# Kernel optimization log

Hardware: AMD Instinct MI355X
Metric: run time of the kernel (lower is better)

Reference implementation:

```python
import jax, jax.numpy as jnp
import numpy as np

N_M, N_H = 50000, 50000
E = 600000
D_IN, D_OUT = 128, 128
LN_EPS = 1e-5
NORM_EPS = 1e-12


def _segment_mean(x, seg, n):
    # PyG 'mean' aggregation: sum / count, 0 for isolated nodes (count clamped to 1)
    s = jax.ops.segment_sum(x, seg, num_segments=n)
    c = jax.ops.segment_sum(jnp.ones((seg.shape[0], 1), x.dtype), seg, num_segments=n)
    return s / jnp.maximum(c, 1.0)


def _sage(t_src, t_dst, ei, Wl, bl, Wr):
    # SAGEConv: lin_l(mean_j x_j) + lin_r(x_i), then L2-normalize rows
    agg = _segment_mean(t_src[ei[0]], ei[1], t_dst.shape[0])
    out = agg @ Wl + bl + t_dst @ Wr
    nrm = jnp.maximum(jnp.linalg.norm(out, axis=-1, keepdims=True), NORM_EPS)
    return out / nrm


def _layer_norm(x, g, b):
    mu = jnp.mean(x, axis=-1, keepdims=True)
    v = jnp.var(x, axis=-1, keepdims=True)
    return (x - mu) / jnp.sqrt(v + LN_EPS) * g + b


def setup_inputs() -> dict:
    key = jax.random.key(0)
    ks = jax.random.split(key, 24)
    r = lambda i, shape: jax.random.normal(ks[i], shape, dtype=jnp.float32) * 0.05
    inp = {
        'x_microbe': jax.random.normal(ks[0], (N_M, D_IN), dtype=jnp.float32),
        'x_host': jax.random.normal(ks[1], (N_H, D_IN), dtype=jnp.float32),
        # per-node-type linear transforms
        'W_nt_m': r(2, (D_IN, D_OUT)), 'b_nt_m': r(3, (D_OUT,)),
        'W_nt_h': r(4, (D_IN, D_OUT)), 'b_nt_h': r(5, (D_OUT,)),
        # SAGEConv params per edge type (lin_l has bias, lin_r has no bias)
        'Wl_mm': r(6, (D_OUT, D_OUT)), 'bl_mm': r(7, (D_OUT,)), 'Wr_mm': r(8, (D_OUT, D_OUT)),
        'Wl_mh': r(9, (D_OUT, D_OUT)), 'bl_mh': r(10, (D_OUT,)), 'Wr_mh': r(11, (D_OUT, D_OUT)),
        'Wl_hm': r(12, (D_OUT, D_OUT)), 'bl_hm': r(13, (D_OUT,)), 'Wr_hm': r(14, (D_OUT, D_OUT)),
        # LayerNorm affine params per node type
        'g_m': jnp.ones((D_OUT,), jnp.float32), 'be_m': jnp.zeros((D_OUT,), jnp.float32),
        'g_h': jnp.ones((D_OUT,), jnp.float32), 'be_h': jnp.zeros((D_OUT,), jnp.float32),
        # edge indices [2, E]: row0 = src, row1 = dst
        'ei_mm': jax.random.randint(ks[15], (2, E), 0, N_M, dtype=jnp.int32),
        'ei_mh': jnp.stack([jax.random.randint(ks[16], (E,), 0, N_M, dtype=jnp.int32),
                            jax.random.randint(ks[17], (E,), 0, N_H, dtype=jnp.int32)]),
        'ei_hm': jnp.stack([jax.random.randint(ks[18], (E,), 0, N_H, dtype=jnp.int32),
                            jax.random.randint(ks[19], (E,), 0, N_M, dtype=jnp.int32)]),
    }
    return inp


def reference(x_microbe, x_host, W_nt_m, b_nt_m, W_nt_h, b_nt_h,
              Wl_mm, bl_mm, Wr_mm, Wl_mh, bl_mh, Wr_mh, Wl_hm, bl_hm, Wr_hm,
              g_m, be_m, g_h, be_h, ei_mm, ei_mh, ei_hm):
    # per-type linear transforms
    t_m = x_microbe @ W_nt_m + b_nt_m
    t_h = x_host @ W_nt_h + b_nt_h
    # SAGEConv per edge type
    o_mm = _sage(t_m, t_m, ei_mm, Wl_mm, bl_mm, Wr_mm)  # microbe -> microbe
    o_mh = _sage(t_m, t_h, ei_mh, Wl_mh, bl_mh, Wr_mh)  # microbe -> host
    o_hm = _sage(t_h, t_m, ei_hm, Wl_hm, bl_hm, Wr_hm)  # host -> microbe
    # HeteroConv aggr='mean' over edge types per dst node type
    conv_m = 0.5 * (o_mm + o_hm)
    conv_h = o_mh
    # residual + LayerNorm (dropout is identity in eval mode)
    out_m = _layer_norm(t_m + conv_m, g_m, be_m)
    out_h = _layer_norm(t_h + conv_h, g_h, be_h)
    return out_m, out_h
```

## Files before the change

### kernel.cpp

```cpp
#include <hip/hip_runtime.h>

typedef unsigned short u16;
typedef unsigned int u32;
typedef __attribute__((ext_vector_type(8))) short bf16x8;
typedef __attribute__((ext_vector_type(4))) float f32x4;

__device__ __forceinline__ float bf_lo(u32 u){ return __uint_as_float(u << 16); }
__device__ __forceinline__ float bf_hi(u32 u){ return __uint_as_float(u & 0xffff0000u); }
__device__ __forceinline__ float bf2f(u16 v){ return __uint_as_float((u32)v << 16); }
__device__ __forceinline__ u16 f2bf(float f){
    u32 u = __float_as_uint(f);
    u32 r = (u + 0x7fffu + ((u >> 16) & 1u)) >> 16;
    return (u16)r;
}
__device__ __forceinline__ u32 pack2(float a, float b){
    return (u32)f2bf(a) | ((u32)f2bf(b) << 16);
}

__global__ __launch_bounds__(256) void fusedA_kernel(
    const int* __restrict__ d0, const int* __restrict__ d1, const int* __restrict__ d2,
    int* __restrict__ rk0, int* __restrict__ rk1, int* __restrict__ rk2,
    int E0, int E1, int E2, int b0, int b1, int b2, int n0, int n1, int n2,
    int* __restrict__ cnt, int h0, int h1, int h2,
    const float* __restrict__ Wf0, const float* __restrict__ Wf1,
    const float* __restrict__ Wf2, const float* __restrict__ Wf3,
    const float* __restrict__ Wf4, const float* __restrict__ Wf5,
    u16* __restrict__ WF,
    const float* __restrict__ Xm, const float* __restrict__ Wm,
    const float* __restrict__ bm, u16* __restrict__ Tm, int NM,
    const float* __restrict__ Xh, const float* __restrict__ Wh,
    const float* __restrict__ bh, u16* __restrict__ Th, int NH,
    int gm, int gh)
{
    int bid = blockIdx.x;
    int HB = h0 + h1 + h2;
    if (bid < HB){
        int t, lb;
        if (bid < h0){ t = 0; lb = bid; }
        else if (bid < h0 + h1){ t = 1; lb = bid - h0; }
        else { t = 2; lb = bid - h0 - h1; }
        const int* d = t == 0 ? d0 : (t == 1 ? d1 : d2);
        int* rk = t == 0 ? rk0 : (t == 1 ? rk1 : rk2);
        int E = t == 0 ? E0 : (t == 1 ? E1 : E2);
        int b = t == 0 ? b0 : (t == 1 ? b1 : b2);
        int n = t == 0 ? n0 : (t == 1 ? n1 : n2);
        int i = lb * 256 + threadIdx.x;
        if (i < E){
            int x = d[i];
            if ((unsigned)x < (unsigned)n) rk[i] = atomicAdd(&cnt[b + x], 1);
        }
        return;
    }
    bid -= HB;
    if (bid < 6){
        const float* W = bid == 0 ? Wf0 : bid == 1 ? Wf1 : bid == 2 ? Wf2 :
                         bid == 3 ? Wf3 : bid == 4 ? Wf4 : Wf5;
        u16* dst = WF + (size_t)bid * 16384;
        #pragma unroll 4
        for (int k = 0; k < 64; ++k){
            int i = k * 256 + threadIdx.x;
            int j   = i & 7;
            int l16 = (i >> 3) & 15;
            int qd  = (i >> 7) & 3;
            int q   = (i >> 9) & 3;
            int tt  = (i >> 11) & 1;
            int w   = (i >> 12) & 3;
            dst[i] = f2bf(W[(q * 32 + qd * 8 + j) * 128 + (w * 32 + tt * 16 + l16)]);
        }
        return;
    }
    bid -= 6;
    const float *A, *W, *bias; u16* C; int N, lgrid, lbid;
    if (bid < gm){ A = Xm; W = Wm; bias = bm; C = Tm; N = NM; lgrid = gm; lbid = bid; }
    else         { A = Xh; W = Wh; bias = bh; C = Th; N = NH; lgrid = gh; lbid = bid - gm; }

    int tid = threadIdx.x;
    int wave = tid >> 6, lane = tid & 63;
    int colHalf = wave & 1;
    int ln16 = lane & 15, quad = lane >> 4;

    bf16x8 Bfrag[4][4];
    #pragma unroll
    for (int t = 0; t < 4; ++t){
        int col = colHalf * 64 + t * 16 + ln16;
        #pragma unroll
        for (int q = 0; q < 4; ++q){
            bf16x8 f;
            #pragma unroll
            for (int j = 0; j < 8; ++j)
                f[j] = (short)f2bf(W[(q * 32 + quad * 8 + j) * 128 + col]);
            Bfrag[t][q] = f;
        }
    }
    float bv[4];
    #pragma unroll
    for (int t = 0; t < 4; ++t)
        bv[t] = bias[colHalf * 64 + t * 16 + ln16];

    int rowBlocks = (N + 15) >> 4;
    for (int rb = lbid * 2 + (wave >> 1); rb < rowBlocks; rb += lgrid * 2){
        int row0 = rb * 16;
        int ar = row0 + ln16; if (ar > N - 1) ar = N - 1;
        const float* Arow = A + (size_t)ar * 128 + quad * 8;
        bf16x8 Af[4];
        #pragma unroll
        for (int q = 0; q < 4; ++q){
            f32x4 lo = *(const f32x4*)(Arow + q * 32);
            f32x4 hi = *(const f32x4*)(Arow + q * 32 + 4);
            bf16x8 f;
            #pragma unroll
            for (int j = 0; j < 4; ++j){ f[j] = (short)f2bf(lo[j]); f[4+j] = (short)f2bf(hi[j]); }
            Af[q] = f;
        }
        f32x4 acc[4];
        #pragma unroll
        for (int t = 0; t < 4; ++t) acc[t] = (f32x4){bv[t], bv[t], bv[t], bv[t]};
        #pragma unroll
        for (int q = 0; q < 4; ++q)
            #pragma unroll
            for (int t = 0; t < 4; ++t)
                acc[t] = __builtin_amdgcn_mfma_f32_16x16x32_bf16(Af[q], Bfrag[t][q], acc[t], 0, 0, 0);
        #pragma unroll
        for (int t = 0; t < 4; ++t){
            int col = colHalf * 64 + t * 16 + ln16;
            #pragma unroll
            for (int r = 0; r < 4; ++r){
                int row = row0 + quad * 4 + r;
                if (row < N) C[(size_t)row * 128 + col] = f2bf(acc[t][r]);
            }
        }
    }
}

__global__ __launch_bounds__(256) void scan_blocks_kernel(
    const int* __restrict__ cnt, int n, int* __restrict__ off, int* __restrict__ part)
{
    __shared__ int lds[256];
    int tid = threadIdx.x;
    int base = blockIdx.x * 2048 + tid * 8;
    int v[8]; int s = 0;
    #pragma unroll
    for (int j = 0; j < 8; ++j){
        int idx = base + j;
        int c = (idx < n) ? cnt[idx] : 0;
        v[j] = s; s += c;
    }
    lds[tid] = s;
    __syncthreads();
    for (int d = 1; d < 256; d <<= 1){
        int t = (tid >= d) ? lds[tid - d] : 0;
        __syncthreads();
        lds[tid] += t;
        __syncthreads();
    }
    int thrBase = (tid > 0) ? lds[tid - 1] : 0;
    if (tid == 255) part[blockIdx.x] = lds[255];
    #pragma unroll
    for (int j = 0; j < 8; ++j){
        int idx = base + j;
        if (idx < n) off[idx] = thrBase + v[j];
    }
}

__global__ __launch_bounds__(128) void scan_part_kernel(
    int* __restrict__ part, int np, int* __restrict__ total_slot)
{
    __shared__ int lds[128];
    int tid = threadIdx.x;
    lds[tid] = (tid < np) ? part[tid] : 0;
    __syncthreads();
    for (int d = 1; d < 128; d <<= 1){
        int t = (tid >= d) ? lds[tid - d] : 0;
        __syncthreads();
        lds[tid] += t;
        __syncthreads();
    }
    if (tid < np) part[tid] = (tid > 0) ? lds[tid - 1] : 0;
    if (tid == 0) *total_slot = lds[np - 1 < 0 ? 0 : np - 1];
}

__global__ __launch_bounds__(256) void scan_add_kernel(
    int* __restrict__ off, const int* __restrict__ part, int n)
{
    int i = blockIdx.x * 256 + threadIdx.x;
    if (i < n) off[i] += part[i >> 11];
}

__global__ __launch_bounds__(256) void fill3_kernel(
    const int* __restrict__ s0, const int* __restrict__ s1, const int* __restrict__ s2,
    const int* __restrict__ d0, const int* __restrict__ d1, const int* __restrict__ d2,
    const int* __restrict__ rk0, const int* __restrict__ rk1, const int* __restrict__ rk2,
    int E0, int E1, int E2, int b0, int b1, int b2, int n0, int n1, int n2,
    const int* __restrict__ off, int* __restrict__ slot)
{
    int t = blockIdx.y;
    int i = blockIdx.x * 256 + threadIdx.x;
    const int* sp = t == 0 ? s0 : (t == 1 ? s1 : s2);
    const int* dp = t == 0 ? d0 : (t == 1 ? d1 : d2);
    const int* rk = t == 0 ? rk0 : (t == 1 ? rk1 : rk2);
    int E = t == 0 ? E0 : (t == 1 ? E1 : E2);
    int b = t == 0 ? b0 : (t == 1 ? b1 : b2);
    int n = t == 0 ? n0 : (t == 1 ? n1 : n2);
    if (i < E){
        int x = dp[i];
        if ((unsigned)x < (unsigned)n){
            slot[off[b + x] + rk[i]] = sp[i];
        }
    }
}

template<int NT>
__global__ __launch_bounds__(256, 4) void sage_ln_kernel(
    const u16* __restrict__ Ts1, const u16* __restrict__ Ts2,
    const u16* __restrict__ Tdst,
    const int* __restrict__ off1, const int* __restrict__ off2,
    const int* __restrict__ slot, int ns1, int ns2,
    const u16* __restrict__ WFl1, const u16* __restrict__ WFr1, const float* __restrict__ bl1,
    const u16* __restrict__ WFl2, const u16* __restrict__ WFr2, const float* __restrict__ bl2,
    const float* __restrict__ g, const float* __restrict__ be,
    float* __restrict__ outp, int N, float scale)
{
    __shared__ u32 aggLDS[NT][16 * 68];
    __shared__ float redN[NT][4][16];
    __shared__ float redS[2][4][16];

    int tid = threadIdx.x;
    int wave = tid >> 6, lane = tid & 63;
    int ln16 = lane & 15, quad = lane >> 4;

    const u16* Ts[2] = {Ts1, Ts2};
    const int* offp[2] = {off1, off2};
    int nsv[2] = {ns1, ns2};
    const u16* WFl[2] = {WFl1, WFl2};
    const u16* WFr[2] = {WFr1, WFr2};
    const float* bls[2] = {bl1, bl2};

    float bv[NT][2];
    #pragma unroll
    for (int et = 0; et < NT; ++et)
        #pragma unroll
        for (int t = 0; t < 2; ++t)
            bv[et][t] = bls[et][wave * 32 + t * 16 + ln16];
    float gv[2], bev[2];
    #pragma unroll
    for (int t = 0; t < 2; ++t){
        int col = wave * 32 + t * 16 + ln16;
        gv[t] = g[col]; bev[t] = be[col];
    }

    int tiles = (N + 15) >> 4;
    for (int tile = blockIdx.x; tile < tiles; tile += gridDim.x){
        int row0 = tile * 16;

        #pragma unroll
        for (int et = 0; et < NT; ++et){
            const u16* Tsrc = Ts[et];
            const int* off = offp[et];
            int n_src = nsv[et];

            int rb[4], rdeg[4], rtake[4], myslot[4];
            #pragma unroll
            for (int r = 0; r < 4; ++r){
                int gg = row0 + wave * 4 + r;
                int b = 0, e = 0;
                if (gg < N){ b = off[gg]; e = off[gg + 1]; }
                rb[r] = b;
                int deg = e - b;
                rdeg[r] = deg;
                int take = deg < 64 ? deg : 64;
                rtake[r] = take;
                int s = 0;
                if (lane < take){
                    s = slot[b + lane];
                    if ((unsigned)s >= (unsigned)n_src) s = 0;
                }
                myslot[r] = s;
            }

            #pragma unroll
            for (int r = 0; r < 4; ++r){
                int lrow = wave * 4 + r;
                float p0 = 0.f, p1 = 0.f, q0 = 0.f, q1 = 0.f;
                float r0 = 0.f, r1 = 0.f, s0 = 0.f, s1 = 0.f;
                int take = rtake[r];
                int j = 0;
                for (; j + 4 <= take; j += 4){
                    int i0 = __shfl(myslot[r], j);
                    int i1 = __shfl(myslot[r], j + 1);
                    int i2 = __shfl(myslot[r], j + 2);
                    int i3 = __shfl(myslot[r], j + 3);
                    u32 u0 = *(const u32*)(Tsrc + (size_t)i0 * 128 + lane * 2);
                    u32 u1 = *(const u32*)(Tsrc + (size_t)i1 * 128 + lane * 2);
                    u32 u2 = *(const u32*)(Tsrc + (size_t)i2 * 128 + lane * 2);
                    u32 u3 = *(const u32*)(Tsrc + (size_t)i3 * 128 + lane * 2);
                    p0 += bf_lo(u0); p1 += bf_hi(u0);
                    q0 += bf_lo(u1); q1 += bf_hi(u1);
                    r0 += bf_lo(u2); r1 += bf_hi(u2);
                    s0 += bf_lo(u3); s1 += bf_hi(u3);
                }
                for (; j < take; ++j){
                    int i0 = __shfl(myslot[r], j);
                    u32 u0 = *(const u32*)(Tsrc + (size_t)i0 * 128 + lane * 2);
                    p0 += bf_lo(u0); p1 += bf_hi(u0);
                }
                for (int j2 = rb[r] + 64; j2 < rb[r] + rdeg[r]; ++j2){
                    int i0 = slot[j2];
                    if ((unsigned)i0 >= (unsigned)n_src) i0 = 0;
                    u32 u0 = *(const u32*)(Tsrc + (size_t)i0 * 128 + lane * 2);
                    p0 += bf_lo(u0); p1 += bf_hi(u0);
                }
                float a0 = (p0 + q0) + (r0 + s0);
                float a1 = (p1 + q1) + (r1 + s1);
                int c = rdeg[r] < 1 ? 1 : rdeg[r];
                float inv = 1.0f / (float)c;
                aggLDS[et][lrow * 68 + lane] = pack2(a0 * inv, a1 * inv);
            }
        }
        __syncthreads();

        int ar = row0 + ln16; if (ar > N - 1) ar = N - 1;
        const u16* Ar2 = Tdst + (size_t)ar * 128 + quad * 8;
        f32x4 acc[NT][2];
        #pragma unroll
        for (int et = 0; et < NT; ++et)
            #pragma unroll
            for (int t = 0; t < 2; ++t)
                acc[et][t] = (f32x4){bv[et][t], bv[et][t], bv[et][t], bv[et][t]};
        #pragma unroll
        for (int q = 0; q < 4; ++q){
            bf16x8 afr = *(const bf16x8*)(Ar2 + q * 32);
            #pragma unroll
            for (int et = 0; et < NT; ++et){
                bf16x8 afl = *(const bf16x8*)&aggLDS[et][ln16 * 68 + q * 16 + quad * 4];
                #pragma unroll
                for (int t = 0; t < 2; ++t){
                    int fo = ((((wave * 2 + t) * 4 + q) * 4 + quad) * 16 + ln16) * 8;
                    bf16x8 BLf = *(const bf16x8*)(WFl[et] + fo);
                    bf16x8 BRf = *(const bf16x8*)(WFr[et] + fo);
                    acc[et][t] = __builtin_amdgcn_mfma_f32_16x16x32_bf16(afl, BLf, acc[et][t], 0, 0, 0);
                    acc[et][t] = __builtin_amdgcn_mfma_f32_16x16x32_bf16(afr, BRf, acc[et][t], 0, 0, 0);
                }
            }
        }

        #pragma unroll
        for (int et = 0; et < NT; ++et){
            #pragma unroll
            for (int r = 0; r < 4; ++r){
                float s = acc[et][0][r] * acc[et][0][r] + acc[et][1][r] * acc[et][1][r];
                #pragma unroll
                for (int m = 1; m < 16; m <<= 1) s += __shfl_xor(s, m);
                if (ln16 == 0) redN[et][wave][quad * 4 + r] = s;
            }
        }
        __syncthreads();

        float yv[2][4];
        float lsum[4], lsq[4];
        #pragma unroll
        for (int r = 0; r < 4; ++r){
            int r16 = quad * 4 + r;
            int row = row0 + r16;
            int crow = row < N ? row : N - 1;
            float sc[NT];
            #pragma unroll
            for (int et = 0; et < NT; ++et){
                float tot = redN[et][0][r16] + redN[et][1][r16] + redN[et][2][r16] + redN[et][3][r16];
                sc[et] = scale / fmaxf(sqrtf(tot), 1e-12f);
            }
            float s1v = 0.f, s2v = 0.f;
            #pragma unroll
            for (int t = 0; t < 2; ++t){
                int col = wave * 32 + t * 16 + ln16;
                float y = bf2f(Tdst[(size_t)crow * 128 + col]);
                #pragma unroll
                for (int et = 0; et < NT; ++et) y += acc[et][t][r] * sc[et];
                yv[t][r] = y;
                s1v += y; s2v += y * y;
            }
            #pragma unroll
            for (int m = 1; m < 16; m <<= 1){ s1v += __shfl_xor(s1v, m); s2v += __shfl_xor(s2v, m); }
            lsum[r] = s1v; lsq[r] = s2v;
        }
        if (ln16 == 0){
            #pragma unroll
            for (int r = 0; r < 4; ++r){
                redS[0][wave][quad * 4 + r] = lsum[r];
                redS[1][wave][quad * 4 + r] = lsq[r];
            }
        }
        __syncthreads();

        #pragma unroll
        for (int r = 0; r < 4; ++r){
            int r16 = quad * 4 + r;
            int row = row0 + r16;
            if (row >= N) continue;
            float S1 = redS[0][0][r16] + redS[0][1][r16] + redS[0][2][r16] + redS[0][3][r16];
            float S2 = redS[1][0][r16] + redS[1][1][r16] + redS[1][2][r16] + redS[1][3][r16];
            float mean = S1 * (1.0f / 128.0f);
            float var = S2 * (1.0f / 128.0f) - mean * mean;
            float rstd = rsqrtf(var + 1e-5f);
            #pragma unroll
            for (int t = 0; t < 2; ++t){
                int col = wave * 32 + t * 16 + ln16;
                outp[(size_t)row * 128 + col] = (yv[t][r] - mean) * rstd * gv[t] + bev[t];
            }
        }
        __syncthreads();
    }
}

extern "C" void kernel_launch(void* const* d_in, const int* in_sizes, int n_in,
                              void* d_out, int out_size, void* d_ws, size_t ws_size,
                              hipStream_t stream) {
    const float* xm    = (const float*)d_in[0];
    const float* xh    = (const float*)d_in[1];
    const float* Wnt_m = (const float*)d_in[2];  const float* bnt_m = (const float*)d_in[3];
    const float* Wnt_h = (const float*)d_in[4];  const float* bnt_h = (const float*)d_in[5];
    const float* Wl_mm = (const float*)d_in[6];  const float* bl_mm = (const float*)d_in[7];
    const float* Wr_mm = (const float*)d_in[8];
    const float* Wl_mh = (const float*)d_in[9];  const float* bl_mh = (const float*)d_in[10];
    const float* Wr_mh = (const float*)d_in[11];
    const float* Wl_hm = (const float*)d_in[12]; const float* bl_hm = (const float*)d_in[13];
    const float* Wr_hm = (const float*)d_in[14];
    const float* g_m   = (const float*)d_in[15]; const float* be_m  = (const float*)d_in[16];
    const float* g_h   = (const float*)d_in[17]; const float* be_h  = (const float*)d_in[18];
    const int* ei_mm = (const int*)d_in[19];
    const int* ei_mh = (const int*)d_in[20];
    const int* ei_hm = (const int*)d_in[21];

    const int D = 128;
    const int NM = in_sizes[0] / D;
    const int NH = in_sizes[1] / D;
    const int E1 = in_sizes[19] / 2;
    const int E2 = in_sizes[20] / 2;
    const int E3 = in_sizes[21] / 2;
    const int Esum = E1 + E2 + E3;
    const int n3 = 2 * NM + NH;

    char* ws = (char*)d_ws;
    size_t woff = 0;
    auto alloc = [&](size_t bytes) -> void* {
        void* p = ws + woff;
        woff += (bytes + 255) & ~(size_t)255;
        return p;
    };
    u16* T_M   = (u16*)alloc((size_t)NM * D * 2);
    u16* T_H   = (u16*)alloc((size_t)NH * D * 2);
    int* CNT3  = (int*)alloc((size_t)n3 * 4);
    int* OFF3  = (int*)alloc((size_t)(n3 + 1) * 4);
    int* SLOT3 = (int*)alloc((size_t)Esum * 4);
    int* PART  = (int*)alloc(1024 * 4);
    u16* WF    = (u16*)alloc((size_t)6 * 16384 * 2);
    if (woff > ws_size) return;

    int* RANK3 = (int*)d_out;
    int* rk0 = RANK3, *rk1 = RANK3 + E1, *rk2 = RANK3 + E1 + E3;

    float* OUT_M = (float*)d_out;
    float* OUT_H = (float*)d_out + (size_t)NM * D;

    const int b0 = 0, b1 = NM, b2 = 2 * NM;
    const int h0 = (E1 + 255) / 256, h1 = (E3 + 255) / 256, h2 = (E2 + 255) / 256;
    const int gm = 1024, gh = 1024;
    int Emax = E1 > E2 ? E1 : E2; if (E3 > Emax) Emax = E3;
    const dim3 egrid((Emax + 255) / 256, 3);
    const int scanBlocks = (n3 + 2047) / 2048;

    hipMemsetAsync(CNT3, 0, (size_t)n3 * 4, stream);

    fusedA_kernel<<<h0 + h1 + h2 + 6 + gm + gh, 256, 0, stream>>>(
        ei_mm + E1, ei_hm + E3, ei_mh + E2,
        rk0, rk1, rk2,
        E1, E3, E2, b0, b1, b2, NM, NM, NH, CNT3, h0, h1, h2,
        Wl_mm, Wr_mm, Wl_hm, Wr_hm, Wl_mh, Wr_mh, WF,
        xm, Wnt_m, bnt_m, T_M, NM,
        xh, Wnt_h, bnt_h, T_H, NH, gm, gh);

    scan_blocks_kernel<<<scanBlocks, 256, 0, stream>>>(CNT3, n3, OFF3, PART);
    scan_part_kernel<<<1, 128, 0, stream>>>(PART, scanBlocks, OFF3 + n3);
    scan_add_kernel<<<(n3 + 255) / 256, 256, 0, stream>>>(OFF3, PART, n3);
    fill3_kernel<<<egrid, 256, 0, stream>>>(
        ei_mm, ei_hm, ei_mh,
        ei_mm + E1, ei_hm + E3, ei_mh + E2,
        rk0, rk1, rk2,
        E1, E3, E2, b0, b1, b2, NM, NM, NH, OFF3, SLOT3);

    sage_ln_kernel<2><<<(NM + 15) / 16, 256, 0, stream>>>(
        T_M, T_H, T_M, OFF3 + b0, OFF3 + b1, SLOT3, NM, NH,
        WF + 0 * 16384, WF + 1 * 16384, bl_mm,
        WF + 2 * 16384, WF + 3 * 16384, bl_hm,
        g_m, be_m, OUT_M, NM, 0.5f);
    sage_ln_kernel<1><<<(NH + 15) / 16, 256, 0, stream>>>(
        T_M, nullptr, T_H, OFF3 + b2, nullptr, SLOT3, NM, 0,
        WF + 4 * 16384, WF + 5 * 16384, bl_mh,
        nullptr, nullptr, nullptr,
        g_h, be_h, OUT_H, NH, 1.0f);
}
```

Before: 541.0 us.

## Split neighbor gather into separate kernel and preload weight fragments in GEMM-LN

The fused gather+GEMM+LayerNorm kernel is split in two. A grid-stride gather kernel computes mean-aggregated bf16 rows for all three edge types into global buffers (the host aggregate temporarily lives in the output buffer). A GEMM+LN kernel then reads those aggregates and keeps all weight fragments in registers, launched persistently with 1024 blocks. This trades an extra global round trip of the aggregates for better load balance, deeper gather unrolling and no LDS staging or barrier between gather and MFMA; register pressure from the preloaded weights may lower occupancy.

```diff
diff --git a/kernel.cpp b/kernel.cpp
--- a/kernel.cpp
+++ b/kernel.cpp
@@ -209,18 +209,97 @@
     }
 }
 
+__global__ __launch_bounds__(256) void gather3_kernel(
+    const u16* __restrict__ TM, const u16* __restrict__ TH,
+    const int* __restrict__ off, const int* __restrict__ slot,
+    u32* __restrict__ AGGM, u32* __restrict__ AGGH, int NM, int NH)
+{
+    int n3 = 2 * NM + NH;
+    int wid = (int)((blockIdx.x * 256u + threadIdx.x) >> 6);
+    int lane = threadIdx.x & 63;
+    int nw = (gridDim.x * 256) >> 6;
+
+    for (int id = wid; id < n3; id += nw){
+        int b = off[id], e = off[id + 1];
+        int deg = e - b;
+        const u16* Tsrc; int nsrc;
+        if (id < NM){ Tsrc = TM; nsrc = NM; }
+        else if (id < 2 * NM){ Tsrc = TH; nsrc = NH; }
+        else { Tsrc = TM; nsrc = NM; }
+
+        int take = deg < 64 ? deg : 64;
+        int ms = 0;
+        if (lane < take){
+            ms = slot[b + lane];
+            if ((unsigned)ms >= (unsigned)nsrc) ms = 0;
+        }
+
+        float a0=0.f,a1=0.f,b0f=0.f,b1f=0.f,c0=0.f,c1=0.f,d0f=0.f,d1f=0.f;
+        float e0=0.f,e1=0.f,f0=0.f,f1=0.f,g0=0.f,g1=0.f,h0=0.f,h1=0.f;
+        int j = 0;
+        for (; j + 8 <= take; j += 8){
+            int i0 = __shfl(ms, j);     int i1 = __shfl(ms, j + 1);
+            int i2 = __shfl(ms, j + 2); int i3 = __shfl(ms, j + 3);
+            int i4 = __shfl(ms, j + 4); int i5 = __shfl(ms, j + 5);
+            int i6 = __shfl(ms, j + 6); int i7 = __shfl(ms, j + 7);
+            u32 u0 = *(const u32*)(Tsrc + (size_t)i0 * 128 + lane * 2);
+            u32 u1 = *(const u32*)(Tsrc + (size_t)i1 * 128 + lane * 2);
+            u32 u2 = *(const u32*)(Tsrc + (size_t)i2 * 128 + lane * 2);
+            u32 u3 = *(const u32*)(Tsrc + (size_t)i3 * 128 + lane * 2);
+            u32 u4 = *(const u32*)(Tsrc + (size_t)i4 * 128 + lane * 2);
+            u32 u5 = *(const u32*)(Tsrc + (size_t)i5 * 128 + lane * 2);
+            u32 u6 = *(const u32*)(Tsrc + (size_t)i6 * 128 + lane * 2);
+            u32 u7 = *(const u32*)(Tsrc + (size_t)i7 * 128 + lane * 2);
+            a0 += bf_lo(u0); a1 += bf_hi(u0);
+            b0f += bf_lo(u1); b1f += bf_hi(u1);
+            c0 += bf_lo(u2); c1 += bf_hi(u2);
+            d0f += bf_lo(u3); d1f += bf_hi(u3);
+            e0 += bf_lo(u4); e1 += bf_hi(u4);
+            f0 += bf_lo(u5); f1 += bf_hi(u5);
+            g0 += bf_lo(u6); g1 += bf_hi(u6);
+            h0 += bf_lo(u7); h1 += bf_hi(u7);
+        }
+        for (; j + 4 <= take; j += 4){
+            int i0 = __shfl(ms, j);     int i1 = __shfl(ms, j + 1);
+            int i2 = __shfl(ms, j + 2); int i3 = __shfl(ms, j + 3);
+            u32 u0 = *(const u32*)(Tsrc + (size_t)i0 * 128 + lane * 2);
+            u32 u1 = *(const u32*)(Tsrc + (size_t)i1 * 128 + lane * 2);
+            u32 u2 = *(const u32*)(Tsrc + (size_t)i2 * 128 + lane * 2);
+            u32 u3 = *(const u32*)(Tsrc + (size_t)i3 * 128 + lane * 2);
+            a0 += bf_lo(u0); a1 += bf_hi(u0);
+            b0f += bf_lo(u1); b1f += bf_hi(u1);
+            c0 += bf_lo(u2); c1 += bf_hi(u2);
+            d0f += bf_lo(u3); d1f += bf_hi(u3);
+        }
+        for (; j < take; ++j){
+            int i0 = __shfl(ms, j);
+            u32 u0 = *(const u32*)(Tsrc + (size_t)i0 * 128 + lane * 2);
+            a0 += bf_lo(u0); a1 += bf_hi(u0);
+        }
+        for (int j2 = b + 64; j2 < e; ++j2){
+            int i0 = slot[j2];
+            if ((unsigned)i0 >= (unsigned)nsrc) i0 = 0;
+            u32 u0 = *(const u32*)(Tsrc + (size_t)i0 * 128 + lane * 2);
+            a0 += bf_lo(u0); a1 += bf_hi(u0);
+        }
+        float s0 = ((a0 + b0f) + (c0 + d0f)) + ((e0 + f0) + (g0 + h0));
+        float s1 = ((a1 + b1f) + (c1 + d1f)) + ((e1 + f1) + (g1 + h1));
+        float inv = 1.0f / (float)(deg < 1 ? 1 : deg);
+        u32 pv = pack2(s0 * inv, s1 * inv);
+        if (id < 2 * NM) AGGM[(size_t)id * 64 + lane] = pv;
+        else             AGGH[(size_t)(id - 2 * NM) * 64 + lane] = pv;
+    }
+}
+
 template<int NT>
-__global__ __launch_bounds__(256, 4) void sage_ln_kernel(
-    const u16* __restrict__ Ts1, const u16* __restrict__ Ts2,
+__global__ __launch_bounds__(256) void gemmln_kernel(
+    const u32* __restrict__ AG1, const u32* __restrict__ AG2,
     const u16* __restrict__ Tdst,
-    const int* __restrict__ off1, const int* __restrict__ off2,
-    const int* __restrict__ slot, int ns1, int ns2,
     const u16* __restrict__ WFl1, const u16* __restrict__ WFr1, const float* __restrict__ bl1,
     const u16* __restrict__ WFl2, const u16* __restrict__ WFr2, const float* __restrict__ bl2,
     const float* __restrict__ g, const float* __restrict__ be,
     float* __restrict__ outp, int N, float scale)
 {
-    __shared__ u32 aggLDS[NT][16 * 68];
     __shared__ float redN[NT][4][16];
     __shared__ float redS[2][4][16];
 
@@ -228,19 +307,26 @@
     int wave = tid >> 6, lane = tid & 63;
     int ln16 = lane & 15, quad = lane >> 4;
 
-    const u16* Ts[2] = {Ts1, Ts2};
-    const int* offp[2] = {off1, off2};
-    int nsv[2] = {ns1, ns2};
+    const u32* AG[2] = {AG1, AG2};
     const u16* WFl[2] = {WFl1, WFl2};
     const u16* WFr[2] = {WFr1, WFr2};
     const float* bls[2] = {bl1, bl2};
 
+    bf16x8 BL[NT][2][4], BR[NT][2][4];
     float bv[NT][2];
     #pragma unroll
-    for (int et = 0; et < NT; ++et)
-        #pragma unroll
-        for (int t = 0; t < 2; ++t)
+    for (int et = 0; et < NT; ++et){
+        #pragma unroll
+        for (int t = 0; t < 2; ++t){
             bv[et][t] = bls[et][wave * 32 + t * 16 + ln16];
+            #pragma unroll
+            for (int q = 0; q < 4; ++q){
+                int fo = ((((wave * 2 + t) * 4 + q) * 4 + quad) * 16 + ln16) * 8;
+                BL[et][t][q] = *(const bf16x8*)(WFl[et] + fo);
+                BR[et][t][q] = *(const bf16x8*)(WFr[et] + fo);
+            }
+        }
+    }
     float gv[2], bev[2];
     #pragma unroll
     for (int t = 0; t < 2; ++t){
@@ -251,94 +337,26 @@
     int tiles = (N + 15) >> 4;
     for (int tile = blockIdx.x; tile < tiles; tile += gridDim.x){
         int row0 = tile * 16;
-
-        #pragma unroll
-        for (int et = 0; et < NT; ++et){
-            const u16* Tsrc = Ts[et];
-            const int* off = offp[et];
-            int n_src = nsv[et];
-
-            int rb[4], rdeg[4], rtake[4], myslot[4];
-            #pragma unroll
-            for (int r = 0; r < 4; ++r){
-                int gg = row0 + wave * 4 + r;
-                int b = 0, e = 0;
-                if (gg < N){ b = off[gg]; e = off[gg + 1]; }
-                rb[r] = b;
-                int deg = e - b;
-                rdeg[r] = deg;
-                int take = deg < 64 ? deg : 64;
-                rtake[r] = take;
-                int s = 0;
-                if (lane < take){
-                    s = slot[b + lane];
-                    if ((unsigned)s >= (unsigned)n_src) s = 0;
-                }
-                myslot[r] = s;
-            }
-
-            #pragma unroll
-            for (int r = 0; r < 4; ++r){
-                int lrow = wave * 4 + r;
-                float p0 = 0.f, p1 = 0.f, q0 = 0.f, q1 = 0.f;
-                float r0 = 0.f, r1 = 0.f, s0 = 0.f, s1 = 0.f;
-                int take = rtake[r];
-                int j = 0;
-                for (; j + 4 <= take; j += 4){
-                    int i0 = __shfl(myslot[r], j);
-                    int i1 = __shfl(myslot[r], j + 1);
-                    int i2 = __shfl(myslot[r], j + 2);
-                    int i3 = __shfl(myslot[r], j + 3);
-                    u32 u0 = *(const u32*)(Tsrc + (size_t)i0 * 128 + lane * 2);
-                    u32 u1 = *(const u32*)(Tsrc + (size_t)i1 * 128 + lane * 2);
-                    u32 u2 = *(const u32*)(Tsrc + (size_t)i2 * 128 + lane * 2);
-                    u32 u3 = *(const u32*)(Tsrc + (size_t)i3 * 128 + lane * 2);
-                    p0 += bf_lo(u0); p1 += bf_hi(u0);
-                    q0 += bf_lo(u1); q1 += bf_hi(u1);
-                    r0 += bf_lo(u2); r1 += bf_hi(u2);
-                    s0 += bf_lo(u3); s1 += bf_hi(u3);
-                }
-                for (; j < take; ++j){
-                    int i0 = __shfl(myslot[r], j);
-                    u32 u0 = *(const u32*)(Tsrc + (size_t)i0 * 128 + lane * 2);
-                    p0 += bf_lo(u0); p1 += bf_hi(u0);
-                }
-                for (int j2 = rb[r] + 64; j2 < rb[r] + rdeg[r]; ++j2){
-                    int i0 = slot[j2];
-                    if ((unsigned)i0 >= (unsigned)n_src) i0 = 0;
-                    u32 u0 = *(const u32*)(Tsrc + (size_t)i0 * 128 + lane * 2);
-                    p0 += bf_lo(u0); p1 += bf_hi(u0);
-                }
-                float a0 = (p0 + q0) + (r0 + s0);
-                float a1 = (p1 + q1) + (r1 + s1);
-                int c = rdeg[r] < 1 ? 1 : rdeg[r];
-                float inv = 1.0f / (float)c;
-                aggLDS[et][lrow * 68 + lane] = pack2(a0 * inv, a1 * inv);
-            }
-        }
-        __syncthreads();
-
         int ar = row0 + ln16; if (ar > N - 1) ar = N - 1;
         const u16* Ar2 = Tdst + (size_t)ar * 128 + quad * 8;
+
         f32x4 acc[NT][2];
         #pragma unroll
         for (int et = 0; et < NT; ++et)
             #pragma unroll
             for (int t = 0; t < 2; ++t)
                 acc[et][t] = (f32x4){bv[et][t], bv[et][t], bv[et][t], bv[et][t]};
+
         #pragma unroll
         for (int q = 0; q < 4; ++q){
             bf16x8 afr = *(const bf16x8*)(Ar2 + q * 32);
             #pragma unroll
             for (int et = 0; et < NT; ++et){
-                bf16x8 afl = *(const bf16x8*)&aggLDS[et][ln16 * 68 + q * 16 + quad * 4];
+                bf16x8 afl = *(const bf16x8*)(AG[et] + (size_t)ar * 64 + q * 16 + quad * 4);
                 #pragma unroll
                 for (int t = 0; t < 2; ++t){
-                    int fo = ((((wave * 2 + t) * 4 + q) * 4 + quad) * 16 + ln16) * 8;
-                    bf16x8 BLf = *(const bf16x8*)(WFl[et] + fo);
-                    bf16x8 BRf = *(const bf16x8*)(WFr[et] + fo);
-                    acc[et][t] = __builtin_amdgcn_mfma_f32_16x16x32_bf16(afl, BLf, acc[et][t], 0, 0, 0);
-                    acc[et][t] = __builtin_amdgcn_mfma_f32_16x16x32_bf16(afr, BRf, acc[et][t], 0, 0, 0);
+                    acc[et][t] = __builtin_amdgcn_mfma_f32_16x16x32_bf16(afl, BL[et][t][q], acc[et][t], 0, 0, 0);
+                    acc[et][t] = __builtin_amdgcn_mfma_f32_16x16x32_bf16(afr, BR[et][t][q], acc[et][t], 0, 0, 0);
                 }
             }
         }
@@ -453,10 +471,12 @@
     int* SLOT3 = (int*)alloc((size_t)Esum * 4);
     int* PART  = (int*)alloc(1024 * 4);
     u16* WF    = (u16*)alloc((size_t)6 * 16384 * 2);
+    u32* AGGM  = (u32*)alloc((size_t)2 * NM * 64 * 4);
     if (woff > ws_size) return;
 
     int* RANK3 = (int*)d_out;
     int* rk0 = RANK3, *rk1 = RANK3 + E1, *rk2 = RANK3 + E1 + E3;
+    u32* AGGH = (u32*)d_out;
 
     float* OUT_M = (float*)d_out;
     float* OUT_H = (float*)d_out + (size_t)NM * D;
@@ -487,14 +507,17 @@
         rk0, rk1, rk2,
         E1, E3, E2, b0, b1, b2, NM, NM, NH, OFF3, SLOT3);
 
-    sage_ln_kernel<2><<<(NM + 15) / 16, 256, 0, stream>>>(
-        T_M, T_H, T_M, OFF3 + b0, OFF3 + b1, SLOT3, NM, NH,
+    gather3_kernel<<<2048, 256, 0, stream>>>(
+        T_M, T_H, OFF3, SLOT3, AGGM, AGGH, NM, NH);
+
+    gemmln_kernel<1><<<1024, 256, 0, stream>>>(
+        AGGH, nullptr, T_H,
+        WF + 4 * 16384, WF + 5 * 16384, bl_mh,
+        nullptr, nullptr, nullptr,
+        g_h, be_h, OUT_H, NH, 1.0f);
+    gemmln_kernel<2><<<1024, 256, 0, stream>>>(
+        AGGM, AGGM + (size_t)NM * 64, T_M,
         WF + 0 * 16384, WF + 1 * 16384, bl_mm,
         WF + 2 * 16384, WF + 3 * 16384, bl_hm,
         g_m, be_m, OUT_M, NM, 0.5f);
-    sage_ln_kernel<1><<<(NH + 15) / 16, 256, 0, stream>>>(
-        T_M, nullptr, T_H, OFF3 + b2, nullptr, SLOT3, NM, 0,
-        WF + 4 * 16384, WF + 5 * 16384, bl_mh,
-        nullptr, nullptr, nullptr,
-        g_h, be_h, OUT_H, NH, 1.0f);
-}
+}
```

Result: faster. 442.4 us (-18.2%).
